# Kernel optimization log

Measured on AMD Instinct MI355X. Metric: run time of the kernel, lower is better.

## Reference

```python
import jax, jax.numpy as jnp
import numpy as np

N = 50000
L = 16            # number of topological levels
PER = N // L      # nodes per level
DEG = 16          # in-degree for non-source nodes
D = 64            # feature dim


def setup_inputs() -> dict:
    key = jax.random.key(0)
    k1, k2, k3 = jax.random.split(key, 3)
    feat = jax.random.normal(k1, (N, D), dtype=jnp.float32)
    delay = jax.random.uniform(k2, (N, D), dtype=jnp.float32)
    intra_delay = jax.random.uniform(k3, (N, D), dtype=jnp.float32)

    # Build a layered DAG: node i has level i // PER; every node with level >= 1
    # receives DEG edges from uniformly random nodes in strictly earlier levels.
    rng = np.random.default_rng(0)
    dst_np = np.repeat(np.arange(PER, N), DEG)               # [E]
    level_start = (dst_np // PER) * PER                      # first node of dst's level
    src_np = np.floor(rng.random(dst_np.shape) * level_start).astype(np.int64)
    node_levels_np = (np.arange(N) // PER).astype(np.int32)

    return {
        "feat": feat,
        "delay": delay,
        "intra_delay": intra_delay,
        "src": jnp.asarray(src_np, dtype=jnp.int32),
        "dst": jnp.asarray(dst_np, dtype=jnp.int32),
        "node_levels": jnp.asarray(node_levels_np, dtype=jnp.int32),
    }


def reference(feat, delay, intra_delay, src, dst, node_levels):
    # Topological propagation (flag_distance=True path):
    #   for each level l = 1..L-1:
    #     m_e        = feat[src_e] + intra_delay[src_e]      (message)
    #     agg_v      = max over incoming edges of m_e        (fn.max reduce)
    #     feat_v     = agg_v + delay_v   for v in level l    (apply node func)
    n = feat.shape[0]
    for l in range(1, L):
        msg = feat[src] + intra_delay[src]                       # [E, D]
        agg = jax.ops.segment_max(msg, dst, num_segments=n)      # [N, D]
        updated = agg + delay                                    # [N, D]
        mask = (node_levels == l)[:, None]                       # [N, 1]
        feat = jnp.where(mask, updated, feat)
    return feat
```

## Files before the change

### kernel.cpp

```cpp
#include <hip/hip_runtime.h>
#include <hip/hip_bf16.h>


#define NN    50000
#define LVL   16
#define PER   3125
#define DEG   16
#define DF    64

#define NBLK  256
#define NTHR  1024
#define NCH   8
#define BPC   32

#define OFF_SLOTS 0
#define OFF_REL   4096
#define OFF_MSGT  8192
#define MSGT_BYTES ((size_t)NN * DF * 4)
#define WS_NEED   (OFF_MSGT + MSGT_BYTES)

__device__ __forceinline__ void st_sc1_f(float* p, float v) {
    __hip_atomic_store(p, v, __ATOMIC_RELAXED, __HIP_MEMORY_SCOPE_AGENT);
}
__device__ __forceinline__ void st_sc1_u(unsigned* p, unsigned v) {
    __hip_atomic_store(p, v, __ATOMIC_RELAXED, __HIP_MEMORY_SCOPE_AGENT);
}
__device__ __forceinline__ unsigned ld_sc1_u(const unsigned* p) {
    return __hip_atomic_load(p, __ATOMIC_RELAXED, __HIP_MEMORY_SCOPE_AGENT);
}

__device__ __forceinline__ void chunk_barrier(unsigned* slots, unsigned* rel,
                                              int rank, unsigned phase) {
    asm volatile("s_barrier" ::: "memory");
    const int w    = threadIdx.x >> 6;
    const int lane = threadIdx.x & 63;
    if (rank == 0) {
        if (w == 0) {
            if (lane == 0) st_sc1_u(&slots[0], phase);
            for (;;) {
                const unsigned v = (lane < BPC) ? ld_sc1_u(&slots[lane]) : phase;
                if (__all(v >= phase)) break;
                __builtin_amdgcn_s_sleep(1);
            }
            if (lane == 0) st_sc1_u(rel, phase);
        }
    } else if (threadIdx.x == 0) {
        st_sc1_u(&slots[rank], phase);
        while (ld_sc1_u(rel) < phase) __builtin_amdgcn_s_sleep(1);
    }
    asm volatile("s_barrier" ::: "memory");
}

__global__ void __launch_bounds__(NTHR) prop_chunk2(
    const float* __restrict__ feat,
    const float* __restrict__ delay,
    const float* __restrict__ intra,
    const int*  __restrict__ src,
    float* __restrict__ out,
    char*  __restrict__ ws)
{
    float* msgT = (float*)(ws + OFF_MSGT);
    const int b     = blockIdx.x;
    const int c     = b & 7;
    const int rank  = b >> 3;
    unsigned* slots = (unsigned*)(ws + OFF_SLOTS) + c * 64;
    unsigned* rel   = (unsigned*)(ws + OFF_REL)  + c * 32;
    const int cbase = c * NN;

    {
        const int i = rank * NTHR + threadIdx.x;
        if (i < PER * 8) {
            const int v = i >> 3, jj = i & 7;
            const int dd = c * 8 + jj;
            st_sc1_f(&msgT[(size_t)(cbase + v) * 8 + jj],
                     feat[(size_t)v * DF + dd] + intra[(size_t)v * DF + dd]);
        }
    }

    const int w    = threadIdx.x >> 6;
    const int lane = threadIdx.x & 63;
    const int n    = lane >> 3, j = lane & 7;
    const int u    = rank * 16 + w;
    const int nv   = u * 8 + n;
    const bool act = (nv < PER);
    const int d    = c * 8 + j;

    float dl = 0.f, it = 0.f;
    if (act) {
        const int v1 = PER + nv;
        dl = delay[(size_t)v1 * DF + d];
        it = intra[(size_t)v1 * DF + d];
        int warm = src[(size_t)(v1 - PER) * DEG + 2 * j];
        asm volatile("" :: "v"(warm));
    }

    asm volatile("s_waitcnt vmcnt(0)" ::: "memory");
    chunk_barrier(slots, rel, rank, 1u);

    for (int l = 1; l < LVL; ++l) {
        float dln = 0.f, itn = 0.f;
        if (act) {
            const int v = l * PER + nv;
            const size_t eb = (size_t)(v - PER) * DEG;
            float m = -INFINITY;
#pragma unroll
            for (int k = 0; k < DEG; ++k) {
                const int s = src[eb + k];
                m = fmaxf(m, msgT[(size_t)(cbase + s) * 8 + j]);
            }
            const float o = m + dl;
            st_sc1_f(&out[(size_t)v * DF + d], o);
            if (l < LVL - 1)
                st_sc1_f(&msgT[(size_t)(cbase + v) * 8 + j], o + it);
            if (l + 1 < LVL) {
                const int vn = (l + 1) * PER + nv;
                dln = delay[(size_t)vn * DF + d];
                itn = intra[(size_t)vn * DF + d];
                int warm = src[(size_t)(vn - PER) * DEG + 2 * j];
                asm volatile("" :: "v"(warm));
            }
        }
        dl = dln; it = itn;
        if (l < LVL - 1) {
            asm volatile("s_waitcnt vmcnt(0)" ::: "memory");
            chunk_barrier(slots, rel, rank, (unsigned)(l + 1));
        }
    }
}

__global__ void __launch_bounds__(256) prop_level(
    float* __restrict__ feat, const float* __restrict__ intra,
    const float* __restrict__ delay, const int* __restrict__ src, int level_start)
{
    const int idx = blockIdx.x * 4 + (threadIdx.x >> 6);
    if (idx >= PER) return;
    const int v = level_start + idx;
    const int d = threadIdx.x & 63;
    const long ebase = (long)(v - PER) * DEG;
    float m = -INFINITY;
#pragma unroll
    for (int k = 0; k < DEG; ++k) {
        const int s = src[ebase + k];
        m = fmaxf(m, feat[(long)s * DF + d] + intra[(long)s * DF + d]);
    }
    feat[(long)v * DF + d] = m + delay[(long)v * DF + d];
}

extern "C" void kernel_launch(void* const* d_in, const int* in_sizes, int n_in,
                              void* d_out, int out_size, void* d_ws, size_t ws_size,
                              hipStream_t stream) {
    const float* feat  = (const float*)d_in[0];
    const float* delay = (const float*)d_in[1];
    const float* intra = (const float*)d_in[2];
    const int*   src   = (const int*)d_in[3];
    float* out = (float*)d_out;

    if (ws_size >= WS_NEED) {
        hipMemsetAsync(d_ws, 0, 8192, stream);
        hipMemcpyAsync(out, feat, (size_t)PER * DF * sizeof(float),
                       hipMemcpyDeviceToDevice, stream);
        prop_chunk2<<<NBLK, NTHR, 0, stream>>>(feat, delay, intra, src, out,
                                               (char*)d_ws);
    } else {
        hipMemcpyAsync(out, feat, (size_t)NN * DF * sizeof(float),
                       hipMemcpyDeviceToDevice, stream);
        const int blocks = (PER + 3) / 4;
        for (int l = 1; l < LVL; ++l)
            prop_level<<<blocks, 256, 0, stream>>>(out, intra, delay, src, l * PER);
    }
}
```

Measured before the change: 92.35 us.

## Use split-arrive counter barrier and prefetch stable-source messages before waiting

Replaces the two-stage leader slot/release barrier with a single monotonic atomic counter per chunk. Each block arrives, then prefetches the next level's source indices, delay and intra values, and the messages from sources already finalized, before it waits. After the wait it reloads only sources from the just-finished level. This hides gather latency behind the barrier wait and removes the leader's poll over all slots. It adds register pressure (16 cached values plus 16 indices) and pads message rows to 16 floats, which doubles the workspace size.

```diff
diff --git a/kernel.cpp b/kernel.cpp
--- a/kernel.cpp
+++ b/kernel.cpp
@@ -12,46 +12,27 @@
 #define NTHR  1024
 #define NCH   8
 #define BPC   32
+#define ROWF  16
 
-#define OFF_SLOTS 0
-#define OFF_REL   4096
+#define OFF_CNT   0
 #define OFF_MSGT  8192
-#define MSGT_BYTES ((size_t)NN * DF * 4)
+#define MSGT_BYTES ((size_t)NN * NCH * ROWF * 4)
 #define WS_NEED   (OFF_MSGT + MSGT_BYTES)
 
 __device__ __forceinline__ void st_sc1_f(float* p, float v) {
-    __hip_atomic_store(p, v, __ATOMIC_RELAXED, __HIP_MEMORY_SCOPE_AGENT);
-}
-__device__ __forceinline__ void st_sc1_u(unsigned* p, unsigned v) {
     __hip_atomic_store(p, v, __ATOMIC_RELAXED, __HIP_MEMORY_SCOPE_AGENT);
 }
 __device__ __forceinline__ unsigned ld_sc1_u(const unsigned* p) {
     return __hip_atomic_load(p, __ATOMIC_RELAXED, __HIP_MEMORY_SCOPE_AGENT);
 }
 
-__device__ __forceinline__ void chunk_barrier(unsigned* slots, unsigned* rel,
-                                              int rank, unsigned phase) {
-    asm volatile("s_barrier" ::: "memory");
-    const int w    = threadIdx.x >> 6;
-    const int lane = threadIdx.x & 63;
-    if (rank == 0) {
-        if (w == 0) {
-            if (lane == 0) st_sc1_u(&slots[0], phase);
-            for (;;) {
-                const unsigned v = (lane < BPC) ? ld_sc1_u(&slots[lane]) : phase;
-                if (__all(v >= phase)) break;
-                __builtin_amdgcn_s_sleep(1);
-            }
-            if (lane == 0) st_sc1_u(rel, phase);
-        }
-    } else if (threadIdx.x == 0) {
-        st_sc1_u(&slots[rank], phase);
-        while (ld_sc1_u(rel) < phase) __builtin_amdgcn_s_sleep(1);
-    }
-    asm volatile("s_barrier" ::: "memory");
-}
+#define UNPACK16(dst, a0, a1, a2, a3)                                   \
+    dst[0]=a0.x; dst[1]=a0.y; dst[2]=a0.z; dst[3]=a0.w;                 \
+    dst[4]=a1.x; dst[5]=a1.y; dst[6]=a1.z; dst[7]=a1.w;                 \
+    dst[8]=a2.x; dst[9]=a2.y; dst[10]=a2.z; dst[11]=a2.w;               \
+    dst[12]=a3.x; dst[13]=a3.y; dst[14]=a3.z; dst[15]=a3.w;
 
-__global__ void __launch_bounds__(NTHR) prop_chunk2(
+__global__ void __launch_bounds__(NTHR) prop_chunk3(
     const float* __restrict__ feat,
     const float* __restrict__ delay,
     const float* __restrict__ intra,
@@ -60,11 +41,10 @@
     char*  __restrict__ ws)
 {
     float* msgT = (float*)(ws + OFF_MSGT);
-    const int b     = blockIdx.x;
-    const int c     = b & 7;
-    const int rank  = b >> 3;
-    unsigned* slots = (unsigned*)(ws + OFF_SLOTS) + c * 64;
-    unsigned* rel   = (unsigned*)(ws + OFF_REL)  + c * 32;
+    const int b    = blockIdx.x;
+    const int c    = b & 7;
+    const int rank = b >> 3;
+    unsigned* cnt  = (unsigned*)(ws + OFF_CNT) + c * 32;
     const int cbase = c * NN;
 
     {
@@ -72,59 +52,89 @@
         if (i < PER * 8) {
             const int v = i >> 3, jj = i & 7;
             const int dd = c * 8 + jj;
-            st_sc1_f(&msgT[(size_t)(cbase + v) * 8 + jj],
+            st_sc1_f(&msgT[(size_t)(cbase + v) * ROWF + jj],
                      feat[(size_t)v * DF + dd] + intra[(size_t)v * DF + dd]);
         }
     }
 
+    const int lane = threadIdx.x & 63;
     const int w    = threadIdx.x >> 6;
-    const int lane = threadIdx.x & 63;
     const int n    = lane >> 3, j = lane & 7;
-    const int u    = rank * 16 + w;
-    const int nv   = u * 8 + n;
+    const int nv   = (rank * 16 + w) * 8 + n;
     const bool act = (nv < PER);
     const int d    = c * 8 + j;
 
+    float g[DEG];
+#pragma unroll
+    for (int k = 0; k < DEG; ++k) g[k] = -INFINITY;
+    int   sidx[DEG];
     float dl = 0.f, it = 0.f;
+
     if (act) {
-        const int v1 = PER + nv;
-        dl = delay[(size_t)v1 * DF + d];
-        it = intra[(size_t)v1 * DF + d];
-        int warm = src[(size_t)(v1 - PER) * DEG + 2 * j];
-        asm volatile("" :: "v"(warm));
+        const int4* sp = (const int4*)(src + (size_t)nv * DEG);
+        int4 a0 = sp[0], a1 = sp[1], a2 = sp[2], a3 = sp[3];
+        UNPACK16(sidx, a0, a1, a2, a3);
+        dl = delay[(size_t)(PER + nv) * DF + d];
+        it = intra[(size_t)(PER + nv) * DF + d];
     }
 
     asm volatile("s_waitcnt vmcnt(0)" ::: "memory");
-    chunk_barrier(slots, rel, rank, 1u);
+    asm volatile("s_barrier" ::: "memory");
+    if (threadIdx.x == 0) {
+        __hip_atomic_fetch_add(cnt, 1u, __ATOMIC_RELAXED,
+                               __HIP_MEMORY_SCOPE_AGENT);
+        while (ld_sc1_u(cnt) < (unsigned)BPC) __builtin_amdgcn_s_sleep(1);
+    }
+    asm volatile("s_barrier" ::: "memory");
 
     for (int l = 1; l < LVL; ++l) {
-        float dln = 0.f, itn = 0.f;
+        const int v       = l * PER + nv;
+        const int lim_old = (l - 1) * PER;
+        float o = 0.f;
         if (act) {
-            const int v = l * PER + nv;
-            const size_t eb = (size_t)(v - PER) * DEG;
+#pragma unroll
+            for (int k = 0; k < DEG; ++k)
+                if (sidx[k] >= lim_old)
+                    g[k] = msgT[(size_t)(cbase + sidx[k]) * ROWF + j];
             float m = -INFINITY;
 #pragma unroll
-            for (int k = 0; k < DEG; ++k) {
-                const int s = src[eb + k];
-                m = fmaxf(m, msgT[(size_t)(cbase + s) * 8 + j]);
-            }
-            const float o = m + dl;
+            for (int k = 0; k < DEG; ++k) m = fmaxf(m, g[k]);
+            o = m + dl;
+            if (l < LVL - 1)
+                st_sc1_f(&msgT[(size_t)(cbase + v) * ROWF + j], o + it);
+        }
+        if (l == LVL - 1) {
+            if (act) st_sc1_f(&out[(size_t)v * DF + d], o);
+            break;
+        }
+
+        asm volatile("s_waitcnt vmcnt(0)" ::: "memory");
+        asm volatile("s_barrier" ::: "memory");
+        if (threadIdx.x == 0)
+            __hip_atomic_fetch_add(cnt, 1u, __ATOMIC_RELAXED,
+                                   __HIP_MEMORY_SCOPE_AGENT);
+
+        if (act) {
             st_sc1_f(&out[(size_t)v * DF + d], o);
-            if (l < LVL - 1)
-                st_sc1_f(&msgT[(size_t)(cbase + v) * 8 + j], o + it);
-            if (l + 1 < LVL) {
-                const int vn = (l + 1) * PER + nv;
-                dln = delay[(size_t)vn * DF + d];
-                itn = intra[(size_t)vn * DF + d];
-                int warm = src[(size_t)(vn - PER) * DEG + 2 * j];
-                asm volatile("" :: "v"(warm));
-            }
+            const int vn = v + PER;
+            const int4* sp = (const int4*)(src + (size_t)(vn - PER) * DEG);
+            int4 a0 = sp[0], a1 = sp[1], a2 = sp[2], a3 = sp[3];
+            UNPACK16(sidx, a0, a1, a2, a3);
+            dl = delay[(size_t)vn * DF + d];
+            it = intra[(size_t)vn * DF + d];
+            const int lim_new = l * PER;
+#pragma unroll
+            for (int k = 0; k < DEG; ++k)
+                g[k] = (sidx[k] < lim_new)
+                     ? msgT[(size_t)(cbase + sidx[k]) * ROWF + j]
+                     : -INFINITY;
         }
-        dl = dln; it = itn;
-        if (l < LVL - 1) {
-            asm volatile("s_waitcnt vmcnt(0)" ::: "memory");
-            chunk_barrier(slots, rel, rank, (unsigned)(l + 1));
+
+        if (threadIdx.x == 0) {
+            const unsigned tgt = (unsigned)((l + 1) * BPC);
+            while (ld_sc1_u(cnt) < tgt) __builtin_amdgcn_s_sleep(1);
         }
+        asm volatile("s_barrier" ::: "memory");
     }
 }
 
@@ -159,7 +169,7 @@
         hipMemsetAsync(d_ws, 0, 8192, stream);
         hipMemcpyAsync(out, feat, (size_t)PER * DF * sizeof(float),
                        hipMemcpyDeviceToDevice, stream);
-        prop_chunk2<<<NBLK, NTHR, 0, stream>>>(feat, delay, intra, src, out,
+        prop_chunk3<<<NBLK, NTHR, 0, stream>>>(feat, delay, intra, src, out,
                                                (char*)d_ws);
     } else {
         hipMemcpyAsync(out, feat, (size_t)NN * DF * sizeof(float),
```

After: 100.3 us. 1.09x slower.
